# Kernel tuning notes

Hardware: AMD Instinct MI355X
Metric: run time of the kernel (lower is better)

Reference implementation:

```python
import jax, jax.numpy as jnp
import numpy as np

NEG_SLOPE = 0.2


def gat_conv(x, src, dst, W, a_src, a_dst, b, concat):
    # x: [N, F_in], src/dst: [E], W: [F_in, H*C], a_src/a_dst: [H, C], b: [H*C] or [C]
    N = x.shape[0]
    H, C = a_src.shape
    h = (x @ W).reshape(N, H, C)                       # [N, H, C]
    s_src = jnp.sum(h * a_src[None], axis=-1)          # [N, H]
    s_dst = jnp.sum(h * a_dst[None], axis=-1)          # [N, H]
    e = jax.nn.leaky_relu(s_src[src] + s_dst[dst], NEG_SLOPE)  # [E, H]
    m = jax.lax.stop_gradient(jax.ops.segment_max(e, dst, num_segments=N))
    ex = jnp.exp(e - m[dst])                           # [E, H]
    denom = jax.ops.segment_sum(ex, dst, num_segments=N)
    alpha = ex / denom[dst]                            # [E, H]
    msg = h[src] * alpha[:, :, None]                   # [E, H, C]
    out = jax.ops.segment_sum(msg, dst, num_segments=N)  # [N, H, C]
    out = out.reshape(N, H * C) if concat else out.mean(axis=1)
    return out + b


def setup_inputs() -> dict:
    key = jax.random.key(0)
    ks = jax.random.split(key, 10)
    N, E, F_IN, HID, HEADS, OUT = 50000, 1600000, 128, 16, 4, 2
    x = jax.random.normal(ks[0], (N, F_IN), dtype=jnp.float32)
    edge_index = jax.random.randint(ks[1], (2, E), 0, N, dtype=jnp.int32)
    W1 = jax.random.normal(ks[2], (F_IN, HEADS * HID), dtype=jnp.float32) / np.sqrt(F_IN)
    att_src1 = jax.random.normal(ks[3], (HEADS, HID), dtype=jnp.float32) / np.sqrt(HID)
    att_dst1 = jax.random.normal(ks[4], (HEADS, HID), dtype=jnp.float32) / np.sqrt(HID)
    b1 = jnp.zeros((HEADS * HID,), dtype=jnp.float32)
    W2 = jax.random.normal(ks[5], (HEADS * HID, OUT), dtype=jnp.float32) / np.sqrt(HEADS * HID)
    att_src2 = jax.random.normal(ks[6], (1, OUT), dtype=jnp.float32)
    att_dst2 = jax.random.normal(ks[7], (1, OUT), dtype=jnp.float32)
    b2 = jnp.zeros((OUT,), dtype=jnp.float32)
    return {"x": x, "edge_index": edge_index, "W1": W1, "att_src1": att_src1,
            "att_dst1": att_dst1, "b1": b1, "W2": W2, "att_src2": att_src2,
            "att_dst2": att_dst2, "b2": b2}


def reference(x, edge_index, W1, att_src1, att_dst1, b1, W2, att_src2, att_dst2, b2):
    N = x.shape[0]
    # PyG GATConv default: add self-loops
    loop = jnp.arange(N, dtype=edge_index.dtype)
    src = jnp.concatenate([edge_index[0], loop])
    dst = jnp.concatenate([edge_index[1], loop])
    # dropout layers are identity at inference
    h = gat_conv(x, src, dst, W1, att_src1, att_dst1, b1, concat=True)
    h = jax.nn.elu(h)
    out = gat_conv(h, src, dst, W2, att_src2, att_dst2, b2, concat=False)
    return jax.nn.log_softmax(out, axis=1)
```

## Files before the change

kernel.cpp:

```cpp
#include <hip/hip_runtime.h>
#include <cstdint>
#include <cstddef>


#define NEG_SLOPE 0.2f
#define BIN_CHUNK 4096
#define CAP 8192

__device__ __forceinline__ float leaky(float v) {
    return v >= 0.f ? v : NEG_SLOPE * v;
}
__device__ __forceinline__ float elu1(float v) {
    return v > 0.f ? v : expm1f(v);
}
__device__ __forceinline__ unsigned short f2bf(float f) {
    unsigned u = __float_as_uint(f);
    u += 0x7fffu + ((u >> 16) & 1u);
    return (unsigned short)(u >> 16);
}
__device__ __forceinline__ float bflo(unsigned u) {
    return __uint_as_float(u << 16);
}
__device__ __forceinline__ float bfhi(unsigned u) {
    return __uint_as_float(u & 0xFFFF0000u);
}

__global__ void init_cursor_kernel(int* __restrict__ cur, int NB) {
    int t = threadIdx.x;
    if (t < NB) cur[t] = t * CAP;
}

__global__ __launch_bounds__(256) void bin_kernel(
    const int* __restrict__ src, const int* __restrict__ dst,
    int* __restrict__ cursor, unsigned* __restrict__ binned,
    int E, int Etot, int NB) {
    __shared__ int hist[512];
    __shared__ int basesh[512];
    for (int i = threadIdx.x; i < NB; i += 256) hist[i] = 0;
    __syncthreads();
    unsigned pk[BIN_CHUNK / 256];
    int base = blockIdx.x * BIN_CHUNK;
#pragma unroll
    for (int k = 0; k < BIN_CHUNK / 256; ++k) {
        int e = base + k * 256 + threadIdx.x;
        pk[k] = 0xFFFFFFFFu;
        if (e < Etot) {
            int s, d;
            if (e < E) { s = src[e]; d = dst[e]; }
            else       { s = d = e - E; }
            pk[k] = ((unsigned)d << 16) | (unsigned)s;
            atomicAdd(&hist[d >> 7], 1);
        }
    }
    __syncthreads();
    for (int i = threadIdx.x; i < NB; i += 256) {
        int c = hist[i];
        basesh[i] = c ? atomicAdd(&cursor[i], c) : 0;
        hist[i] = 0;
    }
    __syncthreads();
#pragma unroll
    for (int k = 0; k < BIN_CHUNK / 256; ++k) {
        if (pk[k] != 0xFFFFFFFFu) {
            int b = pk[k] >> 23;
            int pos = basesh[b] + atomicAdd(&hist[b], 1);
            binned[pos] = pk[k];
        }
    }
}

__global__ __launch_bounds__(256) void csr_build_kernel(
    const unsigned* __restrict__ binned, const int* __restrict__ cursor,
    int2* __restrict__ rng, int* __restrict__ csr, int N, int NB) {
    __shared__ int hist[128];
    __shared__ int sc[128];
    __shared__ int cur[128];
    const int b = blockIdx.x;
    const int base = b * CAP;
    const int endp = cursor[b];
    const int t = threadIdx.x;
    if (t < 128) hist[t] = 0;
    __syncthreads();
    for (int i = base + t; i < endp; i += 256)
        atomicAdd(&hist[(binned[i] >> 16) & 127], 1);
    __syncthreads();
    int v = (t < 128) ? hist[t] : 0;
    if (t < 128) sc[t] = v;
    __syncthreads();
    for (int off = 1; off < 128; off <<= 1) {
        int u = (t >= off && t < 128) ? sc[t - off] : 0;
        __syncthreads();
        if (t < 128) sc[t] += u;
        __syncthreads();
    }
    if (t < 128) {
        int beg = base + sc[t] - v;
        cur[t] = beg;
        int node = b * 128 + t;
        if (node < N) rng[node] = make_int2(beg, beg + v);
    }
    __syncthreads();
    for (int i = base + t; i < endp; i += 256) {
        unsigned p = binned[i];
        int pos = atomicAdd(&cur[(p >> 16) & 127], 1);
        csr[pos] = (int)(p & 0xFFFFu);
    }
}

__global__ __launch_bounds__(256) void gemm1_kernel(
    const float* __restrict__ x, const float* __restrict__ W1,
    const float* __restrict__ a_src, const float* __restrict__ a_dst,
    unsigned short* __restrict__ h1b, float* __restrict__ ssrc1,
    float* __restrict__ sdst1, int N) {
    __shared__ float Ws[128 * 64];
    __shared__ float Xs[32][129];

    const int t = threadIdx.x;
    const int row0 = blockIdx.x * 32;

    for (int i = t * 4; i < 128 * 64; i += 1024) {
        *(float4*)&Ws[i] = *(const float4*)&W1[i];
    }
    for (int i = t * 4; i < 32 * 128; i += 1024) {
        int r = i >> 7, k = i & 127;
        float4 v = make_float4(0.f, 0.f, 0.f, 0.f);
        if (row0 + r < N) v = *(const float4*)&x[(size_t)(row0 + r) * 128 + k];
        Xs[r][k] = v.x; Xs[r][k + 1] = v.y; Xs[r][k + 2] = v.z; Xs[r][k + 3] = v.w;
    }
    __syncthreads();

    const int r0 = (t >> 4) * 2;
    const int c0 = (t & 15) * 4;
    float a00 = 0.f, a01 = 0.f, a02 = 0.f, a03 = 0.f;
    float a10 = 0.f, a11 = 0.f, a12 = 0.f, a13 = 0.f;
#pragma unroll 8
    for (int k = 0; k < 128; ++k) {
        float4 wv = *(const float4*)&Ws[k * 64 + c0];
        float x0 = Xs[r0][k], x1 = Xs[r0 + 1][k];
        a00 = fmaf(x0, wv.x, a00); a01 = fmaf(x0, wv.y, a01);
        a02 = fmaf(x0, wv.z, a02); a03 = fmaf(x0, wv.w, a03);
        a10 = fmaf(x1, wv.x, a10); a11 = fmaf(x1, wv.y, a11);
        a12 = fmaf(x1, wv.z, a12); a13 = fmaf(x1, wv.w, a13);
    }
    const int rowA = row0 + r0, rowB = rowA + 1;
    if (rowA < N) {
        ushort4 pk;
        pk.x = f2bf(a00); pk.y = f2bf(a01); pk.z = f2bf(a02); pk.w = f2bf(a03);
        *(ushort4*)&h1b[(size_t)rowA * 64 + c0] = pk;
    }
    if (rowB < N) {
        ushort4 pk;
        pk.x = f2bf(a10); pk.y = f2bf(a11); pk.z = f2bf(a12); pk.w = f2bf(a13);
        *(ushort4*)&h1b[(size_t)rowB * 64 + c0] = pk;
    }
    float4 av = *(const float4*)&a_src[c0];
    float4 bv = *(const float4*)&a_dst[c0];
    float ps0 = a00 * av.x + a01 * av.y + a02 * av.z + a03 * av.w;
    float pd0 = a00 * bv.x + a01 * bv.y + a02 * bv.z + a03 * bv.w;
    float ps1 = a10 * av.x + a11 * av.y + a12 * av.z + a13 * av.w;
    float pd1 = a10 * bv.x + a11 * bv.y + a12 * bv.z + a13 * bv.w;
    ps0 += __shfl_xor(ps0, 1); ps0 += __shfl_xor(ps0, 2);
    pd0 += __shfl_xor(pd0, 1); pd0 += __shfl_xor(pd0, 2);
    ps1 += __shfl_xor(ps1, 1); ps1 += __shfl_xor(ps1, 2);
    pd1 += __shfl_xor(pd1, 1); pd1 += __shfl_xor(pd1, 2);
    if ((t & 3) == 0) {
        int head = (t & 15) >> 2;
        if (rowA < N) {
            ssrc1[(size_t)rowA * 4 + head] = ps0;
            sdst1[(size_t)rowA * 4 + head] = pd0;
        }
        if (rowB < N) {
            ssrc1[(size_t)rowB * 4 + head] = ps1;
            sdst1[(size_t)rowB * 4 + head] = pd1;
        }
    }
}

__global__ __launch_bounds__(256) void agg1_kernel(
    const int2* __restrict__ rng, const int* __restrict__ csr,
    const float* __restrict__ ssrc1, const float* __restrict__ sdst1,
    const uint4* __restrict__ h1q,
    const float* __restrict__ b1, const float* __restrict__ W2,
    const float* __restrict__ a_src2, const float* __restrict__ a_dst2,
    float4* __restrict__ pk2, float* __restrict__ sdst2, int N) {
    const int lane = threadIdx.x & 63;
    const int d = blockIdx.x * 4 + (threadIdx.x >> 6);
    if (d >= N) return;
    const int2 r = rng[d];
    const int beg = r.x;
    const int cnt = r.y - r.x;
    const int chl = lane & 7;
    const int sub = lane >> 3;
    const int h = chl >> 1;

    const float bh = sdst1[(size_t)d * 4 + h];

    float acc[8] = {0.f, 0.f, 0.f, 0.f, 0.f, 0.f, 0.f, 0.f};
    float den = 0.f;
    int j = sub;
    for (; j + 8 < cnt; j += 16) {
        int s0 = csr[beg + j];
        int s1 = csr[beg + j + 8];
        float sa0 = ssrc1[(size_t)s0 * 4 + h];
        float sa1 = ssrc1[(size_t)s1 * 4 + h];
        uint4 q0 = h1q[(size_t)s0 * 8 + chl];
        uint4 q1 = h1q[(size_t)s1 * 8 + chl];
        float w0 = __expf(leaky(sa0 + bh));
        float w1 = __expf(leaky(sa1 + bh));
        den += w0 + w1;
        acc[0] = fmaf(w0, bflo(q0.x), acc[0]); acc[1] = fmaf(w0, bfhi(q0.x), acc[1]);
        acc[2] = fmaf(w0, bflo(q0.y), acc[2]); acc[3] = fmaf(w0, bfhi(q0.y), acc[3]);
        acc[4] = fmaf(w0, bflo(q0.z), acc[4]); acc[5] = fmaf(w0, bfhi(q0.z), acc[5]);
        acc[6] = fmaf(w0, bflo(q0.w), acc[6]); acc[7] = fmaf(w0, bfhi(q0.w), acc[7]);
        acc[0] = fmaf(w1, bflo(q1.x), acc[0]); acc[1] = fmaf(w1, bfhi(q1.x), acc[1]);
        acc[2] = fmaf(w1, bflo(q1.y), acc[2]); acc[3] = fmaf(w1, bfhi(q1.y), acc[3]);
        acc[4] = fmaf(w1, bflo(q1.z), acc[4]); acc[5] = fmaf(w1, bfhi(q1.z), acc[5]);
        acc[6] = fmaf(w1, bflo(q1.w), acc[6]); acc[7] = fmaf(w1, bfhi(q1.w), acc[7]);
    }
    if (j < cnt) {
        int s0 = csr[beg + j];
        float sa0 = ssrc1[(size_t)s0 * 4 + h];
        uint4 q0 = h1q[(size_t)s0 * 8 + chl];
        float w0 = __expf(leaky(sa0 + bh));
        den += w0;
        acc[0] = fmaf(w0, bflo(q0.x), acc[0]); acc[1] = fmaf(w0, bfhi(q0.x), acc[1]);
        acc[2] = fmaf(w0, bflo(q0.y), acc[2]); acc[3] = fmaf(w0, bfhi(q0.y), acc[3]);
        acc[4] = fmaf(w0, bflo(q0.z), acc[4]); acc[5] = fmaf(w0, bfhi(q0.z), acc[5]);
        acc[6] = fmaf(w0, bflo(q0.w), acc[6]); acc[7] = fmaf(w0, bfhi(q0.w), acc[7]);
    }
#pragma unroll
    for (int off = 8; off <= 32; off <<= 1) {
        den += __shfl_xor(den, off);
#pragma unroll
        for (int i = 0; i < 8; ++i) acc[i] += __shfl_xor(acc[i], off);
    }
    if (sub == 0) {
        const float inv = 1.f / den;
        const int c = chl * 8;
        float p0 = 0.f, p1 = 0.f;
#pragma unroll
        for (int i = 0; i < 8; ++i) {
            float e = elu1(fmaf(acc[i], inv, 0.f) + b1[c + i]);
            p0 = fmaf(e, W2[(c + i) * 2], p0);
            p1 = fmaf(e, W2[(c + i) * 2 + 1], p1);
        }
        p0 += __shfl_xor(p0, 1); p0 += __shfl_xor(p0, 2); p0 += __shfl_xor(p0, 4);
        p1 += __shfl_xor(p1, 1); p1 += __shfl_xor(p1, 2); p1 += __shfl_xor(p1, 4);
        if (chl == 0) {
            float s2 = p0 * a_src2[0] + p1 * a_src2[1];
            float d2 = p0 * a_dst2[0] + p1 * a_dst2[1];
            pk2[d] = make_float4(p0, p1, s2, 0.f);
            sdst2[d] = d2;
        }
    }
}

__global__ __launch_bounds__(256) void agg2_kernel(
    const int2* __restrict__ rng, const int* __restrict__ csr,
    const float4* __restrict__ pk2, const float* __restrict__ sdst2,
    const float* __restrict__ b2, float* __restrict__ out, int N) {
    const int lane = threadIdx.x & 63;
    const int d = blockIdx.x * 4 + (threadIdx.x >> 6);
    if (d >= N) return;
    const int2 r = rng[d];
    const int beg = r.x;
    const int cnt = r.y - r.x;
    const float bs = sdst2[d];

    float den = 0.f, a0 = 0.f, a1 = 0.f;
    int j = lane;
    for (; j + 64 < cnt; j += 128) {
        int s0 = csr[beg + j];
        int s1 = csr[beg + j + 64];
        float4 p0 = pk2[s0];
        float4 p1 = pk2[s1];
        float w0 = __expf(leaky(p0.z + bs));
        float w1 = __expf(leaky(p1.z + bs));
        den += w0 + w1;
        a0 = fmaf(w0, p0.x, a0); a1 = fmaf(w0, p0.y, a1);
        a0 = fmaf(w1, p1.x, a0); a1 = fmaf(w1, p1.y, a1);
    }
    if (j < cnt) {
        int s0 = csr[beg + j];
        float4 p0 = pk2[s0];
        float w0 = __expf(leaky(p0.z + bs));
        den += w0;
        a0 = fmaf(w0, p0.x, a0); a1 = fmaf(w0, p0.y, a1);
    }
#pragma unroll
    for (int off = 1; off <= 32; off <<= 1) {
        den += __shfl_xor(den, off);
        a0  += __shfl_xor(a0, off);
        a1  += __shfl_xor(a1, off);
    }
    if (lane == 0) {
        float z0 = a0 / den + b2[0];
        float z1 = a1 / den + b2[1];
        float mx = fmaxf(z0, z1);
        float lse = mx + logf(__expf(z0 - mx) + __expf(z1 - mx));
        *(float2*)&out[(size_t)d * 2] = make_float2(z0 - lse, z1 - lse);
    }
}

extern "C" void kernel_launch(void* const* d_in, const int* in_sizes, int n_in,
                              void* d_out, int out_size, void* d_ws, size_t ws_size,
                              hipStream_t stream) {
    const float* x   = (const float*)d_in[0];
    const int*   ei  = (const int*)d_in[1];
    const float* W1  = (const float*)d_in[2];
    const float* as1 = (const float*)d_in[3];
    const float* ad1 = (const float*)d_in[4];
    const float* b1  = (const float*)d_in[5];
    const float* W2  = (const float*)d_in[6];
    const float* as2 = (const float*)d_in[7];
    const float* ad2 = (const float*)d_in[8];
    const float* b2  = (const float*)d_in[9];

    const int N    = in_sizes[0] / 128;
    const int E    = in_sizes[1] / 2;
    const int Etot = E + N;
    const int NB   = (N + 127) >> 7;
    const int* src = ei;
    const int* dst = ei + E;

    char* p = (char*)d_ws;
    float4* pk2 = (float4*)p;           p += (size_t)N * 16;
    unsigned short* h1b = (unsigned short*)p; p += (size_t)N * 64 * 2;
    float* ssrc1 = (float*)p;           p += (size_t)N * 4 * 4;
    float* sdst1 = (float*)p;           p += (size_t)N * 4 * 4;
    float* sdst2 = (float*)p;           p += (size_t)N * 4;
    int2* rng    = (int2*)p;            p += (size_t)N * 8;
    int* cursor  = (int*)p;             p += 512 * 4;
    unsigned* binned = (unsigned*)p;    p += (size_t)NB * CAP * 4;
    int* csr     = (int*)p;             p += (size_t)NB * CAP * 4;

    init_cursor_kernel<<<1, 512, 0, stream>>>(cursor, NB);
    const int nbin = (Etot + BIN_CHUNK - 1) / BIN_CHUNK;
    bin_kernel<<<nbin, 256, 0, stream>>>(src, dst, cursor, binned, E, Etot, NB);
    csr_build_kernel<<<NB, 256, 0, stream>>>(binned, cursor, rng, csr, N, NB);

    gemm1_kernel<<<(N + 31) / 32, 256, 0, stream>>>(x, W1, as1, ad1, h1b, ssrc1, sdst1, N);
    agg1_kernel<<<(N + 3) / 4, 256, 0, stream>>>(rng, csr, ssrc1, sdst1,
                                                 (const uint4*)h1b, b1, W2, as2, ad2,
                                                 pk2, sdst2, N);
    agg2_kernel<<<(N + 3) / 4, 256, 0, stream>>>(rng, csr, pk2, sdst2, b2,
                                                 (float*)d_out, N);
}
```

Baseline: 209.5 us.

## Shrink bins to 64 nodes, retile GEMM 4x4, use half-wave per node in aggregation

Bins now hold 64 destination nodes each with a smaller per-bin capacity, and cursors become relative offsets zeroed by a memset instead of an init kernel. The GEMM switches to a transposed X tile with 64 rows per block and a 4x4 register tile per thread, which improves reuse of each shared-memory load. Both aggregation kernels assign 32 lanes per destination node instead of 64, so each block covers 8 nodes and fewer lanes sit idle at the average degree of about 33. The risks are overflowing the smaller per-bin capacity on skewed graphs and extra shared-memory pressure in the GEMM.

```diff
diff --git a/kernel.cpp b/kernel.cpp
--- a/kernel.cpp
+++ b/kernel.cpp
@@ -5,7 +5,7 @@
 
 #define NEG_SLOPE 0.2f
 #define BIN_CHUNK 4096
-#define CAP 8192
+#define CAP 2560
 
 __device__ __forceinline__ float leaky(float v) {
     return v >= 0.f ? v : NEG_SLOPE * v;
@@ -25,17 +25,12 @@
     return __uint_as_float(u & 0xFFFF0000u);
 }
 
-__global__ void init_cursor_kernel(int* __restrict__ cur, int NB) {
-    int t = threadIdx.x;
-    if (t < NB) cur[t] = t * CAP;
-}
-
 __global__ __launch_bounds__(256) void bin_kernel(
     const int* __restrict__ src, const int* __restrict__ dst,
     int* __restrict__ cursor, unsigned* __restrict__ binned,
     int E, int Etot, int NB) {
-    __shared__ int hist[512];
-    __shared__ int basesh[512];
+    __shared__ int hist[800];
+    __shared__ int basesh[800];
     for (int i = threadIdx.x; i < NB; i += 256) hist[i] = 0;
     __syncthreads();
     unsigned pk[BIN_CHUNK / 256];
@@ -49,20 +44,20 @@
             if (e < E) { s = src[e]; d = dst[e]; }
             else       { s = d = e - E; }
             pk[k] = ((unsigned)d << 16) | (unsigned)s;
-            atomicAdd(&hist[d >> 7], 1);
+            atomicAdd(&hist[d >> 6], 1);
         }
     }
     __syncthreads();
     for (int i = threadIdx.x; i < NB; i += 256) {
         int c = hist[i];
-        basesh[i] = c ? atomicAdd(&cursor[i], c) : 0;
+        basesh[i] = c ? (i * CAP + atomicAdd(&cursor[i], c)) : 0;
         hist[i] = 0;
     }
     __syncthreads();
 #pragma unroll
     for (int k = 0; k < BIN_CHUNK / 256; ++k) {
         if (pk[k] != 0xFFFFFFFFu) {
-            int b = pk[k] >> 23;
+            int b = pk[k] >> 22;
             int pos = basesh[b] + atomicAdd(&hist[b], 1);
             binned[pos] = pk[k];
         }
@@ -72,37 +67,37 @@
 __global__ __launch_bounds__(256) void csr_build_kernel(
     const unsigned* __restrict__ binned, const int* __restrict__ cursor,
     int2* __restrict__ rng, int* __restrict__ csr, int N, int NB) {
-    __shared__ int hist[128];
-    __shared__ int sc[128];
-    __shared__ int cur[128];
+    __shared__ int hist[64];
+    __shared__ int sc[64];
+    __shared__ int cur[64];
     const int b = blockIdx.x;
     const int base = b * CAP;
-    const int endp = cursor[b];
+    const int endp = base + cursor[b];
     const int t = threadIdx.x;
-    if (t < 128) hist[t] = 0;
+    if (t < 64) hist[t] = 0;
     __syncthreads();
     for (int i = base + t; i < endp; i += 256)
-        atomicAdd(&hist[(binned[i] >> 16) & 127], 1);
-    __syncthreads();
-    int v = (t < 128) ? hist[t] : 0;
-    if (t < 128) sc[t] = v;
-    __syncthreads();
-    for (int off = 1; off < 128; off <<= 1) {
-        int u = (t >= off && t < 128) ? sc[t - off] : 0;
+        atomicAdd(&hist[(binned[i] >> 16) & 63], 1);
+    __syncthreads();
+    int v = (t < 64) ? hist[t] : 0;
+    if (t < 64) sc[t] = v;
+    __syncthreads();
+    for (int off = 1; off < 64; off <<= 1) {
+        int u = (t >= off && t < 64) ? sc[t - off] : 0;
         __syncthreads();
-        if (t < 128) sc[t] += u;
+        if (t < 64) sc[t] += u;
         __syncthreads();
     }
-    if (t < 128) {
+    if (t < 64) {
         int beg = base + sc[t] - v;
         cur[t] = beg;
-        int node = b * 128 + t;
+        int node = b * 64 + t;
         if (node < N) rng[node] = make_int2(beg, beg + v);
     }
     __syncthreads();
     for (int i = base + t; i < endp; i += 256) {
         unsigned p = binned[i];
-        int pos = atomicAdd(&cur[(p >> 16) & 127], 1);
+        int pos = atomicAdd(&cur[(p >> 16) & 63], 1);
         csr[pos] = (int)(p & 0xFFFFu);
     }
 }
@@ -113,65 +108,64 @@
     unsigned short* __restrict__ h1b, float* __restrict__ ssrc1,
     float* __restrict__ sdst1, int N) {
     __shared__ float Ws[128 * 64];
-    __shared__ float Xs[32][129];
+    __shared__ float Xt[128][69];
 
     const int t = threadIdx.x;
-    const int row0 = blockIdx.x * 32;
+    const int row0 = blockIdx.x * 64;
 
     for (int i = t * 4; i < 128 * 64; i += 1024) {
         *(float4*)&Ws[i] = *(const float4*)&W1[i];
     }
-    for (int i = t * 4; i < 32 * 128; i += 1024) {
+    for (int i = t * 4; i < 64 * 128; i += 1024) {
         int r = i >> 7, k = i & 127;
         float4 v = make_float4(0.f, 0.f, 0.f, 0.f);
         if (row0 + r < N) v = *(const float4*)&x[(size_t)(row0 + r) * 128 + k];
-        Xs[r][k] = v.x; Xs[r][k + 1] = v.y; Xs[r][k + 2] = v.z; Xs[r][k + 3] = v.w;
-    }
-    __syncthreads();
-
-    const int r0 = (t >> 4) * 2;
+        Xt[k][r] = v.x; Xt[k + 1][r] = v.y; Xt[k + 2][r] = v.z; Xt[k + 3][r] = v.w;
+    }
+    __syncthreads();
+
+    const int r0 = (t >> 4) * 4;
     const int c0 = (t & 15) * 4;
-    float a00 = 0.f, a01 = 0.f, a02 = 0.f, a03 = 0.f;
-    float a10 = 0.f, a11 = 0.f, a12 = 0.f, a13 = 0.f;
-#pragma unroll 8
+    float acc[4][4] = {};
+#pragma unroll 4
     for (int k = 0; k < 128; ++k) {
         float4 wv = *(const float4*)&Ws[k * 64 + c0];
-        float x0 = Xs[r0][k], x1 = Xs[r0 + 1][k];
-        a00 = fmaf(x0, wv.x, a00); a01 = fmaf(x0, wv.y, a01);
-        a02 = fmaf(x0, wv.z, a02); a03 = fmaf(x0, wv.w, a03);
-        a10 = fmaf(x1, wv.x, a10); a11 = fmaf(x1, wv.y, a11);
-        a12 = fmaf(x1, wv.z, a12); a13 = fmaf(x1, wv.w, a13);
-    }
-    const int rowA = row0 + r0, rowB = rowA + 1;
-    if (rowA < N) {
-        ushort4 pk;
-        pk.x = f2bf(a00); pk.y = f2bf(a01); pk.z = f2bf(a02); pk.w = f2bf(a03);
-        *(ushort4*)&h1b[(size_t)rowA * 64 + c0] = pk;
-    }
-    if (rowB < N) {
-        ushort4 pk;
-        pk.x = f2bf(a10); pk.y = f2bf(a11); pk.z = f2bf(a12); pk.w = f2bf(a13);
-        *(ushort4*)&h1b[(size_t)rowB * 64 + c0] = pk;
+        float4 xv = *(const float4*)&Xt[k][r0];
+        acc[0][0] = fmaf(xv.x, wv.x, acc[0][0]); acc[0][1] = fmaf(xv.x, wv.y, acc[0][1]);
+        acc[0][2] = fmaf(xv.x, wv.z, acc[0][2]); acc[0][3] = fmaf(xv.x, wv.w, acc[0][3]);
+        acc[1][0] = fmaf(xv.y, wv.x, acc[1][0]); acc[1][1] = fmaf(xv.y, wv.y, acc[1][1]);
+        acc[1][2] = fmaf(xv.y, wv.z, acc[1][2]); acc[1][3] = fmaf(xv.y, wv.w, acc[1][3]);
+        acc[2][0] = fmaf(xv.z, wv.x, acc[2][0]); acc[2][1] = fmaf(xv.z, wv.y, acc[2][1]);
+        acc[2][2] = fmaf(xv.z, wv.z, acc[2][2]); acc[2][3] = fmaf(xv.z, wv.w, acc[2][3]);
+        acc[3][0] = fmaf(xv.w, wv.x, acc[3][0]); acc[3][1] = fmaf(xv.w, wv.y, acc[3][1]);
+        acc[3][2] = fmaf(xv.w, wv.z, acc[3][2]); acc[3][3] = fmaf(xv.w, wv.w, acc[3][3]);
     }
     float4 av = *(const float4*)&a_src[c0];
     float4 bv = *(const float4*)&a_dst[c0];
-    float ps0 = a00 * av.x + a01 * av.y + a02 * av.z + a03 * av.w;
-    float pd0 = a00 * bv.x + a01 * bv.y + a02 * bv.z + a03 * bv.w;
-    float ps1 = a10 * av.x + a11 * av.y + a12 * av.z + a13 * av.w;
-    float pd1 = a10 * bv.x + a11 * bv.y + a12 * bv.z + a13 * bv.w;
-    ps0 += __shfl_xor(ps0, 1); ps0 += __shfl_xor(ps0, 2);
-    pd0 += __shfl_xor(pd0, 1); pd0 += __shfl_xor(pd0, 2);
-    ps1 += __shfl_xor(ps1, 1); ps1 += __shfl_xor(ps1, 2);
-    pd1 += __shfl_xor(pd1, 1); pd1 += __shfl_xor(pd1, 2);
+    float ps[4], pd[4];
+#pragma unroll
+    for (int rr = 0; rr < 4; ++rr) {
+        int row = row0 + r0 + rr;
+        if (row < N) {
+            ushort4 pk;
+            pk.x = f2bf(acc[rr][0]); pk.y = f2bf(acc[rr][1]);
+            pk.z = f2bf(acc[rr][2]); pk.w = f2bf(acc[rr][3]);
+            *(ushort4*)&h1b[(size_t)row * 64 + c0] = pk;
+        }
+        ps[rr] = acc[rr][0] * av.x + acc[rr][1] * av.y + acc[rr][2] * av.z + acc[rr][3] * av.w;
+        pd[rr] = acc[rr][0] * bv.x + acc[rr][1] * bv.y + acc[rr][2] * bv.z + acc[rr][3] * bv.w;
+        ps[rr] += __shfl_xor(ps[rr], 1); ps[rr] += __shfl_xor(ps[rr], 2);
+        pd[rr] += __shfl_xor(pd[rr], 1); pd[rr] += __shfl_xor(pd[rr], 2);
+    }
     if ((t & 3) == 0) {
         int head = (t & 15) >> 2;
-        if (rowA < N) {
-            ssrc1[(size_t)rowA * 4 + head] = ps0;
-            sdst1[(size_t)rowA * 4 + head] = pd0;
-        }
-        if (rowB < N) {
-            ssrc1[(size_t)rowB * 4 + head] = ps1;
-            sdst1[(size_t)rowB * 4 + head] = pd1;
+#pragma unroll
+        for (int rr = 0; rr < 4; ++rr) {
+            int row = row0 + r0 + rr;
+            if (row < N) {
+                ssrc1[(size_t)row * 4 + head] = ps[rr];
+                sdst1[(size_t)row * 4 + head] = pd[rr];
+            }
         }
     }
 }
@@ -183,24 +177,25 @@
     const float* __restrict__ b1, const float* __restrict__ W2,
     const float* __restrict__ a_src2, const float* __restrict__ a_dst2,
     float4* __restrict__ pk2, float* __restrict__ sdst2, int N) {
-    const int lane = threadIdx.x & 63;
-    const int d = blockIdx.x * 4 + (threadIdx.x >> 6);
+    const int tid = threadIdx.x;
+    const int d = blockIdx.x * 8 + (tid >> 5);
     if (d >= N) return;
+    const int l32 = tid & 31;
+    const int sub = l32 >> 3;
+    const int chl = l32 & 7;
+    const int h = chl >> 1;
+
     const int2 r = rng[d];
     const int beg = r.x;
     const int cnt = r.y - r.x;
-    const int chl = lane & 7;
-    const int sub = lane >> 3;
-    const int h = chl >> 1;
-
     const float bh = sdst1[(size_t)d * 4 + h];
 
     float acc[8] = {0.f, 0.f, 0.f, 0.f, 0.f, 0.f, 0.f, 0.f};
     float den = 0.f;
     int j = sub;
-    for (; j + 8 < cnt; j += 16) {
+    for (; j + 4 < cnt; j += 8) {
         int s0 = csr[beg + j];
-        int s1 = csr[beg + j + 8];
+        int s1 = csr[beg + j + 4];
         float sa0 = ssrc1[(size_t)s0 * 4 + h];
         float sa1 = ssrc1[(size_t)s1 * 4 + h];
         uint4 q0 = h1q[(size_t)s0 * 8 + chl];
@@ -229,7 +224,7 @@
         acc[6] = fmaf(w0, bflo(q0.w), acc[6]); acc[7] = fmaf(w0, bfhi(q0.w), acc[7]);
     }
 #pragma unroll
-    for (int off = 8; off <= 32; off <<= 1) {
+    for (int off = 8; off <= 16; off <<= 1) {
         den += __shfl_xor(den, off);
 #pragma unroll
         for (int i = 0; i < 8; ++i) acc[i] += __shfl_xor(acc[i], off);
@@ -240,7 +235,7 @@
         float p0 = 0.f, p1 = 0.f;
 #pragma unroll
         for (int i = 0; i < 8; ++i) {
-            float e = elu1(fmaf(acc[i], inv, 0.f) + b1[c + i]);
+            float e = elu1(acc[i] * inv + b1[c + i]);
             p0 = fmaf(e, W2[(c + i) * 2], p0);
             p1 = fmaf(e, W2[(c + i) * 2 + 1], p1);
         }
@@ -259,19 +254,20 @@
     const int2* __restrict__ rng, const int* __restrict__ csr,
     const float4* __restrict__ pk2, const float* __restrict__ sdst2,
     const float* __restrict__ b2, float* __restrict__ out, int N) {
-    const int lane = threadIdx.x & 63;
-    const int d = blockIdx.x * 4 + (threadIdx.x >> 6);
+    const int tid = threadIdx.x;
+    const int d = blockIdx.x * 8 + (tid >> 5);
     if (d >= N) return;
+    const int l32 = tid & 31;
     const int2 r = rng[d];
     const int beg = r.x;
     const int cnt = r.y - r.x;
     const float bs = sdst2[d];
 
     float den = 0.f, a0 = 0.f, a1 = 0.f;
-    int j = lane;
-    for (; j + 64 < cnt; j += 128) {
+    int j = l32;
+    for (; j + 32 < cnt; j += 64) {
         int s0 = csr[beg + j];
-        int s1 = csr[beg + j + 64];
+        int s1 = csr[beg + j + 32];
         float4 p0 = pk2[s0];
         float4 p1 = pk2[s1];
         float w0 = __expf(leaky(p0.z + bs));
@@ -288,12 +284,12 @@
         a0 = fmaf(w0, p0.x, a0); a1 = fmaf(w0, p0.y, a1);
     }
 #pragma unroll
-    for (int off = 1; off <= 32; off <<= 1) {
+    for (int off = 1; off <= 16; off <<= 1) {
         den += __shfl_xor(den, off);
         a0  += __shfl_xor(a0, off);
         a1  += __shfl_xor(a1, off);
     }
-    if (lane == 0) {
+    if (l32 == 0) {
         float z0 = a0 / den + b2[0];
         float z1 = a1 / den + b2[1];
         float mx = fmaxf(z0, z1);
@@ -319,7 +315,7 @@
     const int N    = in_sizes[0] / 128;
     const int E    = in_sizes[1] / 2;
     const int Etot = E + N;
-    const int NB   = (N + 127) >> 7;
+    const int NB   = (N + 63) >> 6;
     const int* src = ei;
     const int* dst = ei + E;
 
@@ -330,19 +326,19 @@
     float* sdst1 = (float*)p;           p += (size_t)N * 4 * 4;
     float* sdst2 = (float*)p;           p += (size_t)N * 4;
     int2* rng    = (int2*)p;            p += (size_t)N * 8;
-    int* cursor  = (int*)p;             p += 512 * 4;
+    int* cursor  = (int*)p;             p += 1024 * 4;
     unsigned* binned = (unsigned*)p;    p += (size_t)NB * CAP * 4;
     int* csr     = (int*)p;             p += (size_t)NB * CAP * 4;
 
-    init_cursor_kernel<<<1, 512, 0, stream>>>(cursor, NB);
+    hipMemsetAsync(cursor, 0, 1024 * sizeof(int), stream);
+
     const int nbin = (Etot + BIN_CHUNK - 1) / BIN_CHUNK;
     bin_kernel<<<nbin, 256, 0, stream>>>(src, dst, cursor, binned, E, Etot, NB);
     csr_build_kernel<<<NB, 256, 0, stream>>>(binned, cursor, rng, csr, N, NB);
-
-    gemm1_kernel<<<(N + 31) / 32, 256, 0, stream>>>(x, W1, as1, ad1, h1b, ssrc1, sdst1, N);
-    agg1_kernel<<<(N + 3) / 4, 256, 0, stream>>>(rng, csr, ssrc1, sdst1,
+    gemm1_kernel<<<(N + 63) / 64, 256, 0, stream>>>(x, W1, as1, ad1, h1b, ssrc1, sdst1, N);
+    agg1_kernel<<<(N + 7) / 8, 256, 0, stream>>>(rng, csr, ssrc1, sdst1,
                                                  (const uint4*)h1b, b1, W2, as2, ad2,
                                                  pk2, sdst2, N);
-    agg2_kernel<<<(N + 3) / 4, 256, 0, stream>>>(rng, csr, pk2, sdst2, b2,
+    agg2_kernel<<<(N + 7) / 8, 256, 0, stream>>>(rng, csr, pk2, sdst2, b2,
                                                  (float*)d_out, N);
 }
```

New measurement: 197.3 us. -5.8%, faster.
